# Optimization experiments

Measured on AMD Instinct MI355X. Metric: run time of the kernel, lower is better.

The kernel has to match this reference:

```python
import jax, jax.numpy as jnp
import numpy as np

N_NODES = 384
HEIGHT = 60
LN_EPS = 1e-5


def setup_inputs() -> dict:
    key = jax.random.key(0)
    ks = jax.random.split(key, 6)
    C = 256
    E = 3072
    x = jax.random.normal(ks[0], (N_NODES, C, HEIGHT), dtype=jnp.float32)
    edge_attr = jax.random.normal(ks[1], (E, 5), dtype=jnp.float32)
    edge_index = jax.random.randint(ks[2], (2, E), 0, N_NODES)
    W_edge = jax.random.normal(ks[3], (5, C), dtype=jnp.float32) * 0.3
    b_edge = jnp.zeros((C,), dtype=jnp.float32)
    W_conv = jax.random.normal(ks[4], (C, 3 * C), dtype=jnp.float32) * (1.0 / np.sqrt(3 * C))
    ln_gamma = jnp.ones((C, HEIGHT), dtype=jnp.float32)
    ln_beta = jnp.zeros((C, HEIGHT), dtype=jnp.float32)
    return {"x": x, "edge_attr": edge_attr, "edge_index": edge_index,
            "W_edge": W_edge, "b_edge": b_edge, "W_conv": W_conv,
            "ln_gamma": ln_gamma, "ln_beta": ln_beta}


def reference(x, edge_attr, edge_index, W_edge, b_edge, W_conv, ln_gamma, ln_beta):
    # x: (N, C, 60); PyG convention: edge_index[0]=source (j), edge_index[1]=target (i)
    C = x.shape[1]
    src, dst = edge_index[0], edge_index[1]
    h_i = x[dst]                    # (E, C, 60) gather target features
    h_j = x[src]                    # (E, C, 60) gather source features
    ea = edge_attr @ W_edge + b_edge            # (E, C) edge Linear
    ea = jnp.broadcast_to(ea[:, :, None], h_i.shape)  # repeat over height
    h = jnp.concatenate([h_i, h_j - h_i, ea], axis=1)  # (E, 3C, 60)
    # Conv1d kernel_size=1, bias=False -> channel contraction
    m = jnp.einsum('ech,oc->eoh', h, W_conv)    # (E, C, 60)
    # LayerNorm over (C, 60) per edge
    mu = jnp.mean(m, axis=(1, 2), keepdims=True)
    var = jnp.var(m, axis=(1, 2), keepdims=True)
    m = (m - mu) * jax.lax.rsqrt(var + LN_EPS) * ln_gamma + ln_beta
    m = jax.nn.relu(m)
    # aggr='add' scatter into target nodes
    out = jax.ops.segment_sum(m.reshape(m.shape[0], C * HEIGHT), dst,
                              num_segments=N_NODES)
    return out.reshape(N_NODES, C, HEIGHT)
```

## Files before the change

### kernel.cpp

```cpp
#include <hip/hip_runtime.h>

#define N_NODES 384
#define CCH 256
#define HT 60
#define CH (CCH*HT)
#define CH4 (CH/4)
#define LN_EPS 1e-5f

typedef __attribute__((ext_vector_type(8))) short bf16x8;
typedef __attribute__((ext_vector_type(4))) float f32x4;

__device__ inline unsigned short f2bf(float f) {
    unsigned int u = __float_as_uint(f);
    unsigned int r = (u + 0x7FFF + ((u >> 16) & 1)) >> 16;
    return (unsigned short)r;
}
__device__ inline float bf2f(unsigned short u) {
    return __uint_as_float(((unsigned int)u) << 16);
}

__global__ __launch_bounds__(1024) void k_setup(const float* __restrict__ Wc,
                                                unsigned short* __restrict__ Wfrag) {
    int idx = blockIdx.x * 1024 + threadIdx.x;
    int j = idx & 7, lane = (idx >> 3) & 63, ks = (idx >> 9) & 7, mt = idx >> 12;
    int o = mt * 16 + (lane & 15);
    int c = ks * 32 + (lane >> 4) * 8 + j;
    float v;
    if (o < 256) v = Wc[o * 768 + c] - Wc[o * 768 + 256 + c];
    else         v = Wc[(o - 256) * 768 + 256 + c];
    Wfrag[idx] = f2bf(v);
}

__global__ __launch_bounds__(256) void k_node_mfma(const float* __restrict__ x,
                                                   const unsigned short* __restrict__ Wfrag,
                                                   unsigned short* __restrict__ Abf,
                                                   unsigned short* __restrict__ Bbf) {
    __shared__ unsigned short xT[32 * 256];
    int n = blockIdx.x, half = blockIdx.y, tid = threadIdx.x;

    const float4* xg = (const float4*)(x + (size_t)n * CH);
    if (half == 0) {
        for (int i = tid; i < 2048; i += 256) {
            int c = i >> 3, jj = i & 7;
            int r0 = jj * 4;
            float4 v = xg[c * 15 + jj];
            xT[(r0+0) * 256 + (c ^ (((r0+0) & 7) << 3))] = f2bf(v.x);
            xT[(r0+1) * 256 + (c ^ (((r0+1) & 7) << 3))] = f2bf(v.y);
            xT[(r0+2) * 256 + (c ^ (((r0+2) & 7) << 3))] = f2bf(v.z);
            xT[(r0+3) * 256 + (c ^ (((r0+3) & 7) << 3))] = f2bf(v.w);
        }
    } else {
        for (int i = tid; i < 4 * 256; i += 256) {
            int r = 28 + (i >> 8), c = i & 255;
            xT[r * 256 + (c ^ ((r & 7) << 3))] = 0;
        }
        for (int i = tid; i < 1792; i += 256) {
            int c = i / 7, jj = i - c * 7;
            int r0 = jj * 4;
            float4 v = xg[c * 15 + 8 + jj];
            xT[(r0+0) * 256 + (c ^ (((r0+0) & 7) << 3))] = f2bf(v.x);
            xT[(r0+1) * 256 + (c ^ (((r0+1) & 7) << 3))] = f2bf(v.y);
            xT[(r0+2) * 256 + (c ^ (((r0+2) & 7) << 3))] = f2bf(v.z);
            xT[(r0+3) * 256 + (c ^ (((r0+3) & 7) << 3))] = f2bf(v.w);
        }
    }
    __syncthreads();

    int w = tid >> 6, lane = tid & 63;
    int l15 = lane & 15, lg = lane >> 4;

    f32x4 acc[8][2];
#pragma unroll
    for (int mt = 0; mt < 8; ++mt)
#pragma unroll
        for (int nt = 0; nt < 2; ++nt)
            acc[mt][nt] = (f32x4){0.f, 0.f, 0.f, 0.f};

    const unsigned short* wbase = Wfrag + ((size_t)(w * 8) * 8) * 64 * 8;
    for (int ks = 0; ks < 8; ++ks) {
        bf16x8 bfr[2];
#pragma unroll
        for (int nt = 0; nt < 2; ++nt) {
            int row = nt * 16 + l15;
            int col = ks * 32 + lg * 8;
            int idx = row * 256 + (col ^ ((row & 7) << 3));
            bfr[nt] = *(const bf16x8*)(&xT[idx]);
        }
#pragma unroll
        for (int mt = 0; mt < 8; ++mt) {
            const bf16x8 afr = *(const bf16x8*)(wbase + (((size_t)mt * 8 + ks) * 64 + lane) * 8);
#pragma unroll
            for (int nt = 0; nt < 2; ++nt)
                acc[mt][nt] = __builtin_amdgcn_mfma_f32_16x16x32_bf16(afr, bfr[nt], acc[mt][nt], 0, 0, 0);
        }
    }

#pragma unroll
    for (int mt = 0; mt < 8; ++mt) {
        int mtg = w * 8 + mt;
        int obase = mtg * 16 + 4 * lg;
        unsigned short* dst0 = (obase < 256)
            ? (Abf + (size_t)n * CH + (size_t)obase * 60)
            : (Bbf + (size_t)n * CH + (size_t)(obase - 256) * 60);
#pragma unroll
        for (int nt = 0; nt < 2; ++nt) {
            int h = half * 32 + nt * 16 + l15;
            if (h < 60) {
#pragma unroll
                for (int r = 0; r < 4; ++r)
                    dst0[r * 60 + h] = f2bf(acc[mt][nt][r]);
            }
        }
    }
}

__global__ __launch_bounds__(256) void k_prepdots(const unsigned short* __restrict__ Abf,
                                                  const unsigned short* __restrict__ Bbf,
                                                  const float* __restrict__ Wc,
                                                  const float* __restrict__ We,
                                                  const float* __restrict__ be,
                                                  const int* __restrict__ srcA,
                                                  const int* __restrict__ dstA, int E,
                                                  float* __restrict__ RAB,
                                                  float4* __restrict__ Sc,
                                                  float* __restrict__ M,
                                                  float* __restrict__ bias0,
                                                  int* __restrict__ offs,
                                                  int* __restrict__ elist,
                                                  float* __restrict__ Gp8) {
    int b = blockIdx.x;
    int tid = threadIdx.x, w = tid >> 6, lane = tid & 63;
    if (b == 0) {
        __shared__ int cnt[N_NODES];
        __shared__ int sc0[N_NODES], sc1[N_NODES];
        for (int i = tid; i < N_NODES; i += 256) cnt[i] = 0;
        __syncthreads();
        for (int e = tid; e < E; e += 256) atomicAdd(&cnt[dstA[e]], 1);
        __syncthreads();
        for (int i = tid; i < N_NODES; i += 256) sc0[i] = cnt[i];
        __syncthreads();
        int flip = 0;
        for (int d = 1; d < N_NODES; d <<= 1) {
            const int* s_ = flip ? sc1 : sc0;
            int* d_ = flip ? sc0 : sc1;
            for (int i = tid; i < N_NODES; i += 256)
                d_[i] = s_[i] + (i >= d ? s_[i - d] : 0);
            __syncthreads();
            flip ^= 1;
        }
        const int* pos = flip ? sc1 : sc0;
        for (int i = tid; i < N_NODES; i += 256) {
            offs[i + 1] = pos[i];
            cnt[i] = (i == 0) ? 0 : pos[i - 1];
        }
        if (tid == 0) offs[0] = 0;
        __syncthreads();
        for (int e = tid; e < E; e += 256) {
            int d = dstA[e];
            elist[atomicAdd(&cnt[d], 1)] = e;
        }
        __syncthreads();
        for (int n2 = tid; n2 < N_NODES; n2 += 256) {
            int lo = (n2 == 0) ? 0 : pos[n2 - 1], hi = pos[n2];
            for (int i = lo + 1; i < hi; ++i) {
                int key = elist[i]; int j = i - 1;
                while (j >= lo && elist[j] > key) { elist[j + 1] = elist[j]; --j; }
                elist[j + 1] = key;
            }
        }
        return;
    }
    if (b == 1) {
        int o = tid;
        float m0=0,m1=0,m2=0,m3=0,m4=0,bb=0;
        for (int k = 0; k < 256; ++k) {
            float w3 = Wc[o * 768 + 512 + k];
            m0 += We[0*256+k] * w3;
            m1 += We[1*256+k] * w3;
            m2 += We[2*256+k] * w3;
            m3 += We[3*256+k] * w3;
            m4 += We[4*256+k] * w3;
            bb += be[k] * w3;
        }
        M[0*256+o]=m0; M[1*256+o]=m1; M[2*256+o]=m2; M[3*256+o]=m3; M[4*256+o]=m4;
        bias0[o] = bb;
        return;
    }
    if (b < 2 + N_NODES) {
        __shared__ float red[16];
        int n = b - 2;
        const ushort4* Ab = (const ushort4*)(Abf + (size_t)n * CH + tid * 60);
        const ushort4* Bb = (const ushort4*)(Bbf + (size_t)n * CH + tid * 60);
        float rsA = 0.f, qA = 0.f, rsB = 0.f, qB = 0.f;
#pragma unroll
        for (int i = 0; i < 15; ++i) {
            ushort4 a = Ab[i], bb2 = Bb[i];
#pragma unroll
            for (int j = 0; j < 4; ++j) {
                float va = bf2f(((const unsigned short*)&a)[j]);
                float vb = bf2f(((const unsigned short*)&bb2)[j]);
                rsA += va; qA += va * va;
                rsB += vb; qB += vb * vb;
            }
        }
        RAB[(size_t)n * 512 + tid] = rsA;
        RAB[(size_t)n * 512 + 256 + tid] = rsB;
        float sA = rsA, sB = rsB;
#pragma unroll
        for (int o = 32; o >= 1; o >>= 1) {
            sA += __shfl_xor(sA, o, 64); qA += __shfl_xor(qA, o, 64);
            sB += __shfl_xor(sB, o, 64); qB += __shfl_xor(qB, o, 64);
        }
        if (lane == 0) { red[w*4]=sA; red[w*4+1]=qA; red[w*4+2]=sB; red[w*4+3]=qB; }
        __syncthreads();
        if (tid == 0) {
            Sc[n] = make_float4(red[0]+red[4]+red[8]+red[12],
                                red[1]+red[5]+red[9]+red[13],
                                red[2]+red[6]+red[10]+red[14],
                                red[3]+red[7]+red[11]+red[15]);
        }
        return;
    }
    {
        int g = b - (2 + N_NODES);
        int cg8 = g & 7;
        int ew = g >> 3;
        int e = ew * 4 + w;
        if (e >= E) return;
        int s = srcA[e], d = dstA[e];
        const ushort4* Ab = (const ushort4*)(Abf + (size_t)d * CH + (size_t)cg8 * 1920);
        const ushort4* Bb = (const ushort4*)(Bbf + (size_t)s * CH + (size_t)cg8 * 1920);
        float dot = 0.f;
#pragma unroll
        for (int r = 0; r < 7; ++r) {
            int i = lane + 64 * r;
            ushort4 a = Ab[i], bb2 = Bb[i];
            dot += bf2f(a.x) * bf2f(bb2.x) + bf2f(a.y) * bf2f(bb2.y)
                 + bf2f(a.z) * bf2f(bb2.z) + bf2f(a.w) * bf2f(bb2.w);
        }
        if (lane < 32) {
            int i = lane + 448;
            ushort4 a = Ab[i], bb2 = Bb[i];
            dot += bf2f(a.x) * bf2f(bb2.x) + bf2f(a.y) * bf2f(bb2.y)
                 + bf2f(a.z) * bf2f(bb2.z) + bf2f(a.w) * bf2f(bb2.w);
        }
#pragma unroll
        for (int o2 = 32; o2 >= 1; o2 >>= 1)
            dot += __shfl_xor(dot, o2, 64);
        if (lane == 0) Gp8[(size_t)e * 8 + cg8] = dot;
    }
}

__global__ __launch_bounds__(256) void k_stats2(const float* __restrict__ ea,
                                                const float* __restrict__ M,
                                                const float* __restrict__ bias0,
                                                const int* __restrict__ srcA,
                                                const int* __restrict__ dstA, int E,
                                                const float* __restrict__ RAB,
                                                const float4* __restrict__ Sc,
                                                const float* __restrict__ Gp8,
                                                float* __restrict__ cbuf,
                                                float2* __restrict__ stats) {
    int w = threadIdx.x >> 6, lane = threadIdx.x & 63;
    int e = blockIdx.x * 4 + w;
    if (e >= E) return;
    int s = srcA[e], d = dstA[e];
    float ev0 = ea[e*5], ev1 = ea[e*5+1], ev2 = ea[e*5+2], ev3 = ea[e*5+3], ev4 = ea[e*5+4];
    float sc = 0.f, sc2 = 0.f, dots = 0.f;
#pragma unroll
    for (int r = 0; r < 4; ++r) {
        int o = lane + 64 * r;
        float c = bias0[o] + ev0*M[o] + ev1*M[256+o] + ev2*M[512+o] + ev3*M[768+o] + ev4*M[1024+o];
        cbuf[(size_t)e * 256 + o] = c;
        sc += c; sc2 += c * c;
        dots += (RAB[(size_t)d * 512 + o] + RAB[(size_t)s * 512 + 256 + o]) * c;
    }
    float g = (lane < 8) ? Gp8[(size_t)e * 8 + lane] : 0.f;
#pragma unroll
    for (int o2 = 32; o2 >= 1; o2 >>= 1) {
        sc   += __shfl_xor(sc, o2, 64);
        sc2  += __shfl_xor(sc2, o2, 64);
        dots += __shfl_xor(dots, o2, 64);
        g    += __shfl_xor(g, o2, 64);
    }
    if (lane == 0) {
        float4 scd = Sc[d], scs = Sc[s];
        float S1 = scd.x + scs.z + 60.f * sc;
        float S2 = scd.y + scs.w + 60.f * sc2 + 2.f * (g + dots);
        float mu = S1 * (1.0f / (float)CH);
        float var = S2 * (1.0f / (float)CH) - mu * mu;
        stats[e] = make_float2(mu, rsqrtf(var + LN_EPS));
    }
}

__global__ __launch_bounds__(256) void k_apply(const unsigned short* __restrict__ Abf,
                                               const unsigned short* __restrict__ Bbf,
                                               const float* __restrict__ cbuf,
                                               const float2* __restrict__ stats,
                                               const int* __restrict__ srcArr,
                                               const int* __restrict__ offsets,
                                               const int* __restrict__ elist,
                                               const float* __restrict__ gamma,
                                               const float* __restrict__ beta,
                                               float* __restrict__ out) {
    int b = blockIdx.x;
    int cg8 = b & 7;
    int n = b >> 3;
    int tid = threadIdx.x;
    size_t sbase = (size_t)n * CH + (size_t)cg8 * 1920;
    const ushort4* Ab = (const ushort4*)(Abf + sbase);
    const float4*  g4 = (const float4*)(gamma + (size_t)cg8 * 1920);
    const float4*  b4 = (const float4*)(beta  + (size_t)cg8 * 1920);
    bool act1 = (tid < 224);

    float4 af[2], gv[2], bv[2], acc[2];
    int ci[2];
#pragma unroll
    for (int r = 0; r < 2; ++r) {
        acc[r] = make_float4(0.f, 0.f, 0.f, 0.f);
        af[r] = make_float4(0.f, 0.f, 0.f, 0.f);
        gv[r] = make_float4(0.f, 0.f, 0.f, 0.f);
        bv[r] = make_float4(0.f, 0.f, 0.f, 0.f);
        ci[r] = 0;
    }
#pragma unroll
    for (int r = 0; r < 2; ++r) {
        if (r == 0 || act1) {
            int i = tid + 256 * r;
            ci[r] = i / 15;
            ushort4 aw = Ab[i];
            af[r].x = bf2f(aw.x); af[r].y = bf2f(aw.y);
            af[r].z = bf2f(aw.z); af[r].w = bf2f(aw.w);
            gv[r] = g4[i];
            bv[r] = b4[i];
        }
    }

    int lo = offsets[n], hi = offsets[n + 1];
    int k = lo;
    for (; k + 1 < hi; k += 2) {
        int e0 = elist[k], e1 = elist[k + 1];
        int s0 = srcArr[e0], s1 = srcArr[e1];
        float2 st0 = stats[e0], st1 = stats[e1];
        const ushort4* B0 = (const ushort4*)(Bbf + (size_t)s0 * CH + (size_t)cg8 * 1920);
        const ushort4* B1 = (const ushort4*)(Bbf + (size_t)s1 * CH + (size_t)cg8 * 1920);
        const float* c0 = cbuf + (size_t)e0 * 256 + cg8 * 32;
        const float* c1 = cbuf + (size_t)e1 * 256 + cg8 * 32;
#pragma unroll
        for (int r = 0; r < 2; ++r) {
            if (r == 0 || act1) {
                int i = tid + 256 * r;
                ushort4 bw0 = B0[i];
                ushort4 bw1 = B1[i];
                float cc0 = c0[ci[r]];
                float cc1 = c1[ci[r]];
                float m0x = af[r].x + bf2f(bw0.x) + cc0;
                float m0y = af[r].y + bf2f(bw0.y) + cc0;
                float m0z = af[r].z + bf2f(bw0.z) + cc0;
                float m0w = af[r].w + bf2f(bw0.w) + cc0;
                float m1x = af[r].x + bf2f(bw1.x) + cc1;
                float m1y = af[r].y + bf2f(bw1.y) + cc1;
                float m1z = af[r].z + bf2f(bw1.z) + cc1;
                float m1w = af[r].w + bf2f(bw1.w) + cc1;
                acc[r].x += fmaxf((m0x - st0.x) * st0.y * gv[r].x + bv[r].x, 0.f);
                acc[r].y += fmaxf((m0y - st0.x) * st0.y * gv[r].y + bv[r].y, 0.f);
                acc[r].z += fmaxf((m0z - st0.x) * st0.y * gv[r].z + bv[r].z, 0.f);
                acc[r].w += fmaxf((m0w - st0.x) * st0.y * gv[r].w + bv[r].w, 0.f);
                acc[r].x += fmaxf((m1x - st1.x) * st1.y * gv[r].x + bv[r].x, 0.f);
                acc[r].y += fmaxf((m1y - st1.x) * st1.y * gv[r].y + bv[r].y, 0.f);
                acc[r].z += fmaxf((m1z - st1.x) * st1.y * gv[r].z + bv[r].z, 0.f);
                acc[r].w += fmaxf((m1w - st1.x) * st1.y * gv[r].w + bv[r].w, 0.f);
            }
        }
    }
    if (k < hi) {
        int e = elist[k];
        int s = srcArr[e];
        float2 st = stats[e];
        const ushort4* Bb = (const ushort4*)(Bbf + (size_t)s * CH + (size_t)cg8 * 1920);
        const float* cc = cbuf + (size_t)e * 256 + cg8 * 32;
#pragma unroll
        for (int r = 0; r < 2; ++r) {
            if (r == 0 || act1) {
                int i = tid + 256 * r;
                float ccv = cc[ci[r]];
                ushort4 bw = Bb[i];
                float mx = af[r].x + bf2f(bw.x) + ccv;
                float my = af[r].y + bf2f(bw.y) + ccv;
                float mz = af[r].z + bf2f(bw.z) + ccv;
                float mw = af[r].w + bf2f(bw.w) + ccv;
                acc[r].x += fmaxf((mx - st.x) * st.y * gv[r].x + bv[r].x, 0.f);
                acc[r].y += fmaxf((my - st.x) * st.y * gv[r].y + bv[r].y, 0.f);
                acc[r].z += fmaxf((mz - st.x) * st.y * gv[r].z + bv[r].z, 0.f);
                acc[r].w += fmaxf((mw - st.x) * st.y * gv[r].w + bv[r].w, 0.f);
            }
        }
    }
    float4* ob = (float4*)(out + sbase);
#pragma unroll
    for (int r = 0; r < 2; ++r)
        if (r == 0 || act1) ob[tid + 256 * r] = acc[r];
}

extern "C" void kernel_launch(void* const* d_in, const int* in_sizes, int n_in,
                              void* d_out, int out_size, void* d_ws, size_t ws_size,
                              hipStream_t stream) {
    const float* x     = (const float*)d_in[0];
    const float* ea    = (const float*)d_in[1];
    const int*   ei    = (const int*)d_in[2];
    const float* We    = (const float*)d_in[3];
    const float* be    = (const float*)d_in[4];
    const float* Wc    = (const float*)d_in[5];
    const float* gamma = (const float*)d_in[6];
    const float* beta  = (const float*)d_in[7];
    const int E = in_sizes[2] / 2;
    const int* src = ei;
    const int* dst = ei + E;

    char* ws = (char*)d_ws;
    size_t off = 0;
    auto alloc = [&](size_t bytes) -> void* {
        void* p = ws + off;
        off += (bytes + 255) & ~(size_t)255;
        return p;
    };
    unsigned short* Abf    = (unsigned short*)alloc((size_t)N_NODES * CH * 2);
    unsigned short* Bbf    = (unsigned short*)alloc((size_t)N_NODES * CH * 2);
    float*          cbuf   = (float*)alloc((size_t)E * 256 * 4);
    float2*         stats  = (float2*)alloc((size_t)E * 8);
    unsigned short* Wfrag  = (unsigned short*)alloc(512 * 256 * 2);
    float*          M      = (float*)alloc(5 * 256 * 4);
    float*          bias0  = (float*)alloc(256 * 4);
    float*          RAB    = (float*)alloc((size_t)N_NODES * 512 * 4);
    float4*         Sc     = (float4*)alloc((size_t)N_NODES * 16);
    float*          Gp8    = (float*)alloc((size_t)E * 8 * 4);
    int*            offs   = (int*)alloc((N_NODES + 1) * 4);
    int*            elist  = (int*)alloc((size_t)E * 4);

    int ndot = ((E + 3) / 4) * 8;
    k_setup<<<128, 1024, 0, stream>>>(Wc, Wfrag);
    k_node_mfma<<<dim3(N_NODES, 2), 256, 0, stream>>>(x, Wfrag, Abf, Bbf);
    k_prepdots<<<2 + N_NODES + ndot, 256, 0, stream>>>(Abf, Bbf, Wc, We, be, src, dst, E,
                                                       RAB, Sc, M, bias0, offs, elist, Gp8);
    k_stats2<<<(E + 3) / 4, 256, 0, stream>>>(ea, M, bias0, src, dst, E, RAB, Sc, Gp8,
                                              cbuf, stats);
    k_apply<<<N_NODES * 8, 256, 0, stream>>>(Abf, Bbf, cbuf, stats, src, offs, elist,
                                             gamma, beta, (float*)d_out);
}
```

Baseline: 85.06 us.

## Eliminate stats kernel by precomputing projected scalars and computing LN stats in apply

Removes the separate k_stats2 launch. The M/bias0 projection and its scalar Gram terms move into an extra k_setup block, per-node projections of row sums onto M are computed in k_prepdots, and cbuf is written there too. k_apply now rebuilds each edge's LayerNorm mean and rstd from these precomputed scalars in chunks held in shared memory. This drops one launch and the RAB/stats round trip, at the cost of redundant per-edge stats work in each of the 8 channel-group blocks and extra barriers.

```diff
diff --git a/kernel.cpp b/kernel.cpp
--- a/kernel.cpp
+++ b/kernel.cpp
@@ -6,6 +6,7 @@
 #define CH (CCH*HT)
 #define CH4 (CH/4)
 #define LN_EPS 1e-5f
+#define CHK 96
 
 typedef __attribute__((ext_vector_type(8))) short bf16x8;
 typedef __attribute__((ext_vector_type(4))) float f32x4;
@@ -20,15 +21,67 @@
 }
 
 __global__ __launch_bounds__(1024) void k_setup(const float* __restrict__ Wc,
-                                                unsigned short* __restrict__ Wfrag) {
-    int idx = blockIdx.x * 1024 + threadIdx.x;
-    int j = idx & 7, lane = (idx >> 3) & 63, ks = (idx >> 9) & 7, mt = idx >> 12;
-    int o = mt * 16 + (lane & 15);
-    int c = ks * 32 + (lane >> 4) * 8 + j;
-    float v;
-    if (o < 256) v = Wc[o * 768 + c] - Wc[o * 768 + 256 + c];
-    else         v = Wc[(o - 256) * 768 + 256 + c];
-    Wfrag[idx] = f2bf(v);
+                                                const float* __restrict__ We,
+                                                const float* __restrict__ be,
+                                                unsigned short* __restrict__ Wfrag,
+                                                float* __restrict__ M,
+                                                float* __restrict__ bias0,
+                                                float* __restrict__ Scal) {
+    __shared__ float Ml[5 * 256];
+    __shared__ float bl[256];
+    int tid = threadIdx.x;
+    if (blockIdx.x < 128) {
+        int idx = blockIdx.x * 1024 + tid;
+        int j = idx & 7, lane = (idx >> 3) & 63, ks = (idx >> 9) & 7, mt = idx >> 12;
+        int o = mt * 16 + (lane & 15);
+        int c = ks * 32 + (lane >> 4) * 8 + j;
+        float v;
+        if (o < 256) v = Wc[o * 768 + c] - Wc[o * 768 + 256 + c];
+        else         v = Wc[(o - 256) * 768 + 256 + c];
+        Wfrag[idx] = f2bf(v);
+        return;
+    }
+    if (tid < 256) {
+        int o = tid;
+        float m0=0,m1=0,m2=0,m3=0,m4=0,bb=0;
+        for (int k = 0; k < 256; ++k) {
+            float w3 = Wc[o * 768 + 512 + k];
+            m0 += We[0*256+k] * w3;
+            m1 += We[1*256+k] * w3;
+            m2 += We[2*256+k] * w3;
+            m3 += We[3*256+k] * w3;
+            m4 += We[4*256+k] * w3;
+            bb += be[k] * w3;
+        }
+        M[0*256+o]=m0; M[1*256+o]=m1; M[2*256+o]=m2; M[3*256+o]=m3; M[4*256+o]=m4;
+        bias0[o] = bb;
+        Ml[0*256+o]=m0; Ml[1*256+o]=m1; Ml[2*256+o]=m2; Ml[3*256+o]=m3; Ml[4*256+o]=m4;
+        bl[o] = bb;
+    }
+    __syncthreads();
+    if (tid < 256) {
+        int w = tid >> 6, lane = tid & 63;
+        for (int q = w; q < 37; q += 4) {
+            float s = 0.f;
+#pragma unroll
+            for (int r = 0; r < 4; ++r) {
+                int o = lane + 64 * r;
+                float v;
+                if (q < 5)       v = Ml[q * 256 + o];
+                else if (q == 5) v = bl[o];
+                else if (q < 11) v = Ml[(q - 6) * 256 + o] * bl[o];
+                else if (q == 11) v = bl[o] * bl[o];
+                else {
+                    int t = q - 12, j = t / 5, k = t % 5;
+                    v = Ml[j * 256 + o] * Ml[k * 256 + o];
+                }
+                s += v;
+            }
+#pragma unroll
+            for (int o2 = 32; o2 >= 1; o2 >>= 1) s += __shfl_xor(s, o2, 64);
+            if (lane == 0) Scal[q] = s;
+        }
+    }
 }
 
 __global__ __launch_bounds__(256) void k_node_mfma(const float* __restrict__ x,
@@ -116,18 +169,17 @@
 
 __global__ __launch_bounds__(256) void k_prepdots(const unsigned short* __restrict__ Abf,
                                                   const unsigned short* __restrict__ Bbf,
-                                                  const float* __restrict__ Wc,
-                                                  const float* __restrict__ We,
-                                                  const float* __restrict__ be,
+                                                  const float* __restrict__ ea,
+                                                  const float* __restrict__ M,
+                                                  const float* __restrict__ bias0,
                                                   const int* __restrict__ srcA,
                                                   const int* __restrict__ dstA, int E,
-                                                  float* __restrict__ RAB,
                                                   float4* __restrict__ Sc,
-                                                  float* __restrict__ M,
-                                                  float* __restrict__ bias0,
+                                                  float* __restrict__ NodeProj,
                                                   int* __restrict__ offs,
                                                   int* __restrict__ elist,
-                                                  float* __restrict__ Gp8) {
+                                                  float* __restrict__ EPd,
+                                                  float* __restrict__ cbuf) {
     int b = blockIdx.x;
     int tid = threadIdx.x, w = tid >> 6, lane = tid & 63;
     if (b == 0) {
@@ -170,25 +222,10 @@
         }
         return;
     }
-    if (b == 1) {
-        int o = tid;
-        float m0=0,m1=0,m2=0,m3=0,m4=0,bb=0;
-        for (int k = 0; k < 256; ++k) {
-            float w3 = Wc[o * 768 + 512 + k];
-            m0 += We[0*256+k] * w3;
-            m1 += We[1*256+k] * w3;
-            m2 += We[2*256+k] * w3;
-            m3 += We[3*256+k] * w3;
-            m4 += We[4*256+k] * w3;
-            bb += be[k] * w3;
-        }
-        M[0*256+o]=m0; M[1*256+o]=m1; M[2*256+o]=m2; M[3*256+o]=m3; M[4*256+o]=m4;
-        bias0[o] = bb;
-        return;
-    }
-    if (b < 2 + N_NODES) {
+    if (b < 1 + N_NODES) {
         __shared__ float red[16];
-        int n = b - 2;
+        __shared__ float rA[256], rB[256];
+        int n = b - 1;
         const ushort4* Ab = (const ushort4*)(Abf + (size_t)n * CH + tid * 60);
         const ushort4* Bb = (const ushort4*)(Bbf + (size_t)n * CH + tid * 60);
         float rsA = 0.f, qA = 0.f, rsB = 0.f, qB = 0.f;
@@ -203,8 +240,7 @@
                 rsB += vb; qB += vb * vb;
             }
         }
-        RAB[(size_t)n * 512 + tid] = rsA;
-        RAB[(size_t)n * 512 + 256 + tid] = rsB;
+        rA[tid] = rsA; rB[tid] = rsB;
         float sA = rsA, sB = rsB;
 #pragma unroll
         for (int o = 32; o >= 1; o >>= 1) {
@@ -219,15 +255,38 @@
                                 red[2]+red[6]+red[10]+red[14],
                                 red[3]+red[7]+red[11]+red[15]);
         }
+        for (int q = w; q < 12; q += 4) {
+            float s = 0.f;
+#pragma unroll
+            for (int r = 0; r < 4; ++r) {
+                int o = lane + 64 * r;
+                float coef = (q == 5 || q == 11) ? bias0[o] : M[((q < 5) ? q : q - 6) * 256 + o];
+                float rv = (q < 6) ? rA[o] : rB[o];
+                s += rv * coef;
+            }
+#pragma unroll
+            for (int o2 = 32; o2 >= 1; o2 >>= 1) s += __shfl_xor(s, o2, 64);
+            if (lane == 0) NodeProj[(size_t)n * 12 + q] = s;
+        }
         return;
     }
     {
-        int g = b - (2 + N_NODES);
+        int g = b - (1 + N_NODES);
         int cg8 = g & 7;
         int ew = g >> 3;
         int e = ew * 4 + w;
         if (e >= E) return;
         int s = srcA[e], d = dstA[e];
+
+        if (lane < 32) {
+            int o = cg8 * 32 + lane;
+            float ev0 = ea[e*5], ev1 = ea[e*5+1], ev2 = ea[e*5+2],
+                  ev3 = ea[e*5+3], ev4 = ea[e*5+4];
+            float c = bias0[o] + ev0*M[o] + ev1*M[256+o] + ev2*M[512+o]
+                    + ev3*M[768+o] + ev4*M[1024+o];
+            cbuf[(size_t)e * 256 + o] = c;
+        }
+
         const ushort4* Ab = (const ushort4*)(Abf + (size_t)d * CH + (size_t)cg8 * 1920);
         const ushort4* Bb = (const ushort4*)(Bbf + (size_t)s * CH + (size_t)cg8 * 1920);
         float dot = 0.f;
@@ -247,71 +306,40 @@
 #pragma unroll
         for (int o2 = 32; o2 >= 1; o2 >>= 1)
             dot += __shfl_xor(dot, o2, 64);
-        if (lane == 0) Gp8[(size_t)e * 8 + cg8] = dot;
-    }
-}
-
-__global__ __launch_bounds__(256) void k_stats2(const float* __restrict__ ea,
-                                                const float* __restrict__ M,
-                                                const float* __restrict__ bias0,
-                                                const int* __restrict__ srcA,
-                                                const int* __restrict__ dstA, int E,
-                                                const float* __restrict__ RAB,
-                                                const float4* __restrict__ Sc,
-                                                const float* __restrict__ Gp8,
-                                                float* __restrict__ cbuf,
-                                                float2* __restrict__ stats) {
-    int w = threadIdx.x >> 6, lane = threadIdx.x & 63;
-    int e = blockIdx.x * 4 + w;
-    if (e >= E) return;
-    int s = srcA[e], d = dstA[e];
-    float ev0 = ea[e*5], ev1 = ea[e*5+1], ev2 = ea[e*5+2], ev3 = ea[e*5+3], ev4 = ea[e*5+4];
-    float sc = 0.f, sc2 = 0.f, dots = 0.f;
-#pragma unroll
-    for (int r = 0; r < 4; ++r) {
-        int o = lane + 64 * r;
-        float c = bias0[o] + ev0*M[o] + ev1*M[256+o] + ev2*M[512+o] + ev3*M[768+o] + ev4*M[1024+o];
-        cbuf[(size_t)e * 256 + o] = c;
-        sc += c; sc2 += c * c;
-        dots += (RAB[(size_t)d * 512 + o] + RAB[(size_t)s * 512 + 256 + o]) * c;
-    }
-    float g = (lane < 8) ? Gp8[(size_t)e * 8 + lane] : 0.f;
-#pragma unroll
-    for (int o2 = 32; o2 >= 1; o2 >>= 1) {
-        sc   += __shfl_xor(sc, o2, 64);
-        sc2  += __shfl_xor(sc2, o2, 64);
-        dots += __shfl_xor(dots, o2, 64);
-        g    += __shfl_xor(g, o2, 64);
-    }
-    if (lane == 0) {
-        float4 scd = Sc[d], scs = Sc[s];
-        float S1 = scd.x + scs.z + 60.f * sc;
-        float S2 = scd.y + scs.w + 60.f * sc2 + 2.f * (g + dots);
-        float mu = S1 * (1.0f / (float)CH);
-        float var = S2 * (1.0f / (float)CH) - mu * mu;
-        stats[e] = make_float2(mu, rsqrtf(var + LN_EPS));
+        if (lane == 0) EPd[(size_t)e * 8 + cg8] = dot;
     }
 }
 
 __global__ __launch_bounds__(256) void k_apply(const unsigned short* __restrict__ Abf,
                                                const unsigned short* __restrict__ Bbf,
                                                const float* __restrict__ cbuf,
-                                               const float2* __restrict__ stats,
+                                               const float* __restrict__ EPd,
+                                               const float4* __restrict__ Sc,
+                                               const float* __restrict__ NodeProj,
+                                               const float* __restrict__ Scal,
+                                               const float* __restrict__ ea,
                                                const int* __restrict__ srcArr,
                                                const int* __restrict__ offsets,
                                                const int* __restrict__ elist,
                                                const float* __restrict__ gamma,
                                                const float* __restrict__ beta,
                                                float* __restrict__ out) {
+    __shared__ float2 stl[CHK];
     int b = blockIdx.x;
     int cg8 = b & 7;
     int n = b >> 3;
-    int tid = threadIdx.x;
+    int tid = threadIdx.x, w = tid >> 6, lane = tid & 63;
     size_t sbase = (size_t)n * CH + (size_t)cg8 * 1920;
     const ushort4* Ab = (const ushort4*)(Abf + sbase);
     const float4*  g4 = (const float4*)(gamma + (size_t)cg8 * 1920);
     const float4*  b4 = (const float4*)(beta  + (size_t)cg8 * 1920);
     bool act1 = (tid < 224);
+
+    float4 scd = Sc[n];
+    float PA0n = NodeProj[(size_t)n * 12 + 5];
+    float Pn0 = NodeProj[(size_t)n * 12 + 0], Pn1 = NodeProj[(size_t)n * 12 + 1],
+          Pn2 = NodeProj[(size_t)n * 12 + 2], Pn3 = NodeProj[(size_t)n * 12 + 3],
+          Pn4 = NodeProj[(size_t)n * 12 + 4];
 
     float4 af[2], gv[2], bv[2], acc[2];
     int ci[2];
@@ -337,62 +365,100 @@
     }
 
     int lo = offsets[n], hi = offsets[n + 1];
-    int k = lo;
-    for (; k + 1 < hi; k += 2) {
-        int e0 = elist[k], e1 = elist[k + 1];
-        int s0 = srcArr[e0], s1 = srcArr[e1];
-        float2 st0 = stats[e0], st1 = stats[e1];
-        const ushort4* B0 = (const ushort4*)(Bbf + (size_t)s0 * CH + (size_t)cg8 * 1920);
-        const ushort4* B1 = (const ushort4*)(Bbf + (size_t)s1 * CH + (size_t)cg8 * 1920);
-        const float* c0 = cbuf + (size_t)e0 * 256 + cg8 * 32;
-        const float* c1 = cbuf + (size_t)e1 * 256 + cg8 * 32;
-#pragma unroll
-        for (int r = 0; r < 2; ++r) {
-            if (r == 0 || act1) {
-                int i = tid + 256 * r;
-                ushort4 bw0 = B0[i];
-                ushort4 bw1 = B1[i];
-                float cc0 = c0[ci[r]];
-                float cc1 = c1[ci[r]];
-                float m0x = af[r].x + bf2f(bw0.x) + cc0;
-                float m0y = af[r].y + bf2f(bw0.y) + cc0;
-                float m0z = af[r].z + bf2f(bw0.z) + cc0;
-                float m0w = af[r].w + bf2f(bw0.w) + cc0;
-                float m1x = af[r].x + bf2f(bw1.x) + cc1;
-                float m1y = af[r].y + bf2f(bw1.y) + cc1;
-                float m1z = af[r].z + bf2f(bw1.z) + cc1;
-                float m1w = af[r].w + bf2f(bw1.w) + cc1;
-                acc[r].x += fmaxf((m0x - st0.x) * st0.y * gv[r].x + bv[r].x, 0.f);
-                acc[r].y += fmaxf((m0y - st0.x) * st0.y * gv[r].y + bv[r].y, 0.f);
-                acc[r].z += fmaxf((m0z - st0.x) * st0.y * gv[r].z + bv[r].z, 0.f);
-                acc[r].w += fmaxf((m0w - st0.x) * st0.y * gv[r].w + bv[r].w, 0.f);
-                acc[r].x += fmaxf((m1x - st1.x) * st1.y * gv[r].x + bv[r].x, 0.f);
-                acc[r].y += fmaxf((m1y - st1.x) * st1.y * gv[r].y + bv[r].y, 0.f);
-                acc[r].z += fmaxf((m1z - st1.x) * st1.y * gv[r].z + bv[r].z, 0.f);
-                acc[r].w += fmaxf((m1w - st1.x) * st1.y * gv[r].w + bv[r].w, 0.f);
-            }
-        }
-    }
-    if (k < hi) {
-        int e = elist[k];
-        int s = srcArr[e];
-        float2 st = stats[e];
-        const ushort4* Bb = (const ushort4*)(Bbf + (size_t)s * CH + (size_t)cg8 * 1920);
-        const float* cc = cbuf + (size_t)e * 256 + cg8 * 32;
-#pragma unroll
-        for (int r = 0; r < 2; ++r) {
-            if (r == 0 || act1) {
-                int i = tid + 256 * r;
-                float ccv = cc[ci[r]];
-                ushort4 bw = Bb[i];
-                float mx = af[r].x + bf2f(bw.x) + ccv;
-                float my = af[r].y + bf2f(bw.y) + ccv;
-                float mz = af[r].z + bf2f(bw.z) + ccv;
-                float mw = af[r].w + bf2f(bw.w) + ccv;
-                acc[r].x += fmaxf((mx - st.x) * st.y * gv[r].x + bv[r].x, 0.f);
-                acc[r].y += fmaxf((my - st.x) * st.y * gv[r].y + bv[r].y, 0.f);
-                acc[r].z += fmaxf((mz - st.x) * st.y * gv[r].z + bv[r].z, 0.f);
-                acc[r].w += fmaxf((mw - st.x) * st.y * gv[r].w + bv[r].w, 0.f);
+    for (int base = lo; base < hi; base += CHK) {
+        int cnt = min(CHK, hi - base);
+        if (base != lo) __syncthreads();
+        for (int kk = w; kk < cnt; kk += 4) {
+            int e = elist[base + kk];
+            int s = srcArr[e];
+            float dot = 0.f;
+            if (lane < 8) dot = EPd[(size_t)e * 8 + lane];
+            dot += __shfl_xor(dot, 4, 64);
+            dot += __shfl_xor(dot, 2, 64);
+            dot += __shfl_xor(dot, 1, 64);
+            if (lane == 0) {
+                float e0 = ea[e*5], e1 = ea[e*5+1], e2 = ea[e*5+2],
+                      e3 = ea[e*5+3], e4 = ea[e*5+4];
+                float sumc = Scal[5] + e0*Scal[0] + e1*Scal[1] + e2*Scal[2]
+                           + e3*Scal[3] + e4*Scal[4];
+                float sumc2 = Scal[11]
+                    + 2.f * (e0*Scal[6] + e1*Scal[7] + e2*Scal[8] + e3*Scal[9] + e4*Scal[10]);
+                float ev[5] = {e0, e1, e2, e3, e4};
+#pragma unroll
+                for (int j = 0; j < 5; ++j)
+#pragma unroll
+                    for (int k2 = 0; k2 < 5; ++k2)
+                        sumc2 += ev[j] * ev[k2] * Scal[12 + j * 5 + k2];
+                const float* nps = NodeProj + (size_t)s * 12;
+                float dots = PA0n + e0*Pn0 + e1*Pn1 + e2*Pn2 + e3*Pn3 + e4*Pn4
+                           + nps[11] + e0*nps[6] + e1*nps[7] + e2*nps[8]
+                           + e3*nps[9] + e4*nps[10];
+                float4 scs = Sc[s];
+                float S1 = scd.x + scs.z + 60.f * sumc;
+                float S2 = scd.y + scs.w + 60.f * sumc2 + 2.f * (dot + dots);
+                float mu = S1 * (1.0f / (float)CH);
+                float var = S2 * (1.0f / (float)CH) - mu * mu;
+                stl[kk] = make_float2(mu, rsqrtf(var + LN_EPS));
+            }
+        }
+        __syncthreads();
+        int k = 0;
+        for (; k + 1 < cnt; k += 2) {
+            int e0 = elist[base + k], e1 = elist[base + k + 1];
+            int s0 = srcArr[e0], s1 = srcArr[e1];
+            float2 st0 = stl[k], st1 = stl[k + 1];
+            const ushort4* B0 = (const ushort4*)(Bbf + (size_t)s0 * CH + (size_t)cg8 * 1920);
+            const ushort4* B1 = (const ushort4*)(Bbf + (size_t)s1 * CH + (size_t)cg8 * 1920);
+            const float* c0 = cbuf + (size_t)e0 * 256 + cg8 * 32;
+            const float* c1 = cbuf + (size_t)e1 * 256 + cg8 * 32;
+#pragma unroll
+            for (int r = 0; r < 2; ++r) {
+                if (r == 0 || act1) {
+                    int i = tid + 256 * r;
+                    ushort4 bw0 = B0[i];
+                    ushort4 bw1 = B1[i];
+                    float cc0 = c0[ci[r]];
+                    float cc1 = c1[ci[r]];
+                    float m0x = af[r].x + bf2f(bw0.x) + cc0;
+                    float m0y = af[r].y + bf2f(bw0.y) + cc0;
+                    float m0z = af[r].z + bf2f(bw0.z) + cc0;
+                    float m0w = af[r].w + bf2f(bw0.w) + cc0;
+                    float m1x = af[r].x + bf2f(bw1.x) + cc1;
+                    float m1y = af[r].y + bf2f(bw1.y) + cc1;
+                    float m1z = af[r].z + bf2f(bw1.z) + cc1;
+                    float m1w = af[r].w + bf2f(bw1.w) + cc1;
+                    acc[r].x += fmaxf((m0x - st0.x) * st0.y * gv[r].x + bv[r].x, 0.f);
+                    acc[r].y += fmaxf((m0y - st0.x) * st0.y * gv[r].y + bv[r].y, 0.f);
+                    acc[r].z += fmaxf((m0z - st0.x) * st0.y * gv[r].z + bv[r].z, 0.f);
+                    acc[r].w += fmaxf((m0w - st0.x) * st0.y * gv[r].w + bv[r].w, 0.f);
+                    acc[r].x += fmaxf((m1x - st1.x) * st1.y * gv[r].x + bv[r].x, 0.f);
+                    acc[r].y += fmaxf((m1y - st1.x) * st1.y * gv[r].y + bv[r].y, 0.f);
+                    acc[r].z += fmaxf((m1z - st1.x) * st1.y * gv[r].z + bv[r].z, 0.f);
+                    acc[r].w += fmaxf((m1w - st1.x) * st1.y * gv[r].w + bv[r].w, 0.f);
+                }
+            }
+        }
+        if (k < cnt) {
+            int e = elist[base + k];
+            int s = srcArr[e];
+            float2 st = stl[k];
+            const ushort4* Bb = (const ushort4*)(Bbf + (size_t)s * CH + (size_t)cg8 * 1920);
+            const float* cc = cbuf + (size_t)e * 256 + cg8 * 32;
+#pragma unroll
+            for (int r = 0; r < 2; ++r) {
+                if (r == 0 || act1) {
+                    int i = tid + 256 * r;
+                    float ccv = cc[ci[r]];
+                    ushort4 bw = Bb[i];
+                    float mx = af[r].x + bf2f(bw.x) + ccv;
+                    float my = af[r].y + bf2f(bw.y) + ccv;
+                    float mz = af[r].z + bf2f(bw.z) + ccv;
+                    float mw = af[r].w + bf2f(bw.w) + ccv;
+                    acc[r].x += fmaxf((mx - st.x) * st.y * gv[r].x + bv[r].x, 0.f);
+                    acc[r].y += fmaxf((my - st.x) * st.y * gv[r].y + bv[r].y, 0.f);
+                    acc[r].z += fmaxf((mz - st.x) * st.y * gv[r].z + bv[r].z, 0.f);
+                    acc[r].w += fmaxf((mw - st.x) * st.y * gv[r].w + bv[r].w, 0.f);
+                }
             }
         }
     }
@@ -427,23 +493,21 @@
     unsigned short* Abf    = (unsigned short*)alloc((size_t)N_NODES * CH * 2);
     unsigned short* Bbf    = (unsigned short*)alloc((size_t)N_NODES * CH * 2);
     float*          cbuf   = (float*)alloc((size_t)E * 256 * 4);
-    float2*         stats  = (float2*)alloc((size_t)E * 8);
     unsigned short* Wfrag  = (unsigned short*)alloc(512 * 256 * 2);
     float*          M      = (float*)alloc(5 * 256 * 4);
     float*          bias0  = (float*)alloc(256 * 4);
-    float*          RAB    = (float*)alloc((size_t)N_NODES * 512 * 4);
+    float*          Scal   = (float*)alloc(64 * 4);
     float4*         Sc     = (float4*)alloc((size_t)N_NODES * 16);
-    float*          Gp8    = (float*)alloc((size_t)E * 8 * 4);
+    float*          NodeProj = (float*)alloc((size_t)N_NODES * 12 * 4);
+    float*          EPd    = (float*)alloc((size_t)E * 8 * 4);
     int*            offs   = (int*)alloc((N_NODES + 1) * 4);
     int*            elist  = (int*)alloc((size_t)E * 4);
 
     int ndot = ((E + 3) / 4) * 8;
-    k_setup<<<128, 1024, 0, stream>>>(Wc, Wfrag);
+    k_setup<<<129, 1024, 0, stream>>>(Wc, We, be, Wfrag, M, bias0, Scal);
     k_node_mfma<<<dim3(N_NODES, 2), 256, 0, stream>>>(x, Wfrag, Abf, Bbf);
-    k_prepdots<<<2 + N_NODES + ndot, 256, 0, stream>>>(Abf, Bbf, Wc, We, be, src, dst, E,
-                                                       RAB, Sc, M, bias0, offs, elist, Gp8);
-    k_stats2<<<(E + 3) / 4, 256, 0, stream>>>(ea, M, bias0, src, dst, E, RAB, Sc, Gp8,
-                                              cbuf, stats);
-    k_apply<<<N_NODES * 8, 256, 0, stream>>>(Abf, Bbf, cbuf, stats, src, offs, elist,
-                                             gamma, beta, (float*)d_out);
-}
+    k_prepdots<<<1 + N_NODES + ndot, 256, 0, stream>>>(Abf, Bbf, ea, M, bias0, src, dst, E,
+                                                       Sc, NodeProj, offs, elist, EPd, cbuf);
+    k_apply<<<N_NODES * 8, 256, 0, stream>>>(Abf, Bbf, cbuf, EPd, Sc, NodeProj, Scal, ea,
+                                             src, offs, elist, gamma, beta, (float*)d_out);
+}
```

Result: slower. 112.1 us (+31.8%).
